# Performance work log

Measured on AMD Instinct MI355X. Metric: run time of the kernel, lower is better.

The kernel has to match this reference:

```python
import jax, jax.numpy as jnp
import numpy as np

N = 100000    # nodes ('paper')
E = 600000    # edges per relation
R = 3         # relations (etypes)
IN = 256      # in_feats
HF = 256      # h_feats
H = 4         # n_heads
D = HF // H   # per-head dim
C = 153       # num_classes
NEG_SLOPE = 0.2


def setup_inputs() -> dict:
    key = jax.random.key(0)
    ks = jax.random.split(key, 14)
    s = 0.05
    x = jax.random.normal(ks[0], (N, IN), jnp.float32)
    src = jax.random.randint(ks[1], (R, E), 0, N, jnp.int32)
    dst = jax.random.randint(ks[2], (R, E), 0, N, jnp.int32)
    # layer 1 params (per relation): fc weight, attn_l, attn_r, bias
    W1 = jax.random.normal(ks[3], (R, IN, HF), jnp.float32) * s
    al1 = jax.random.normal(ks[4], (R, H, D), jnp.float32) * s
    ar1 = jax.random.normal(ks[5], (R, H, D), jnp.float32) * s
    b1 = jax.random.normal(ks[6], (R, HF), jnp.float32) * s
    # layer 2 params
    W2 = jax.random.normal(ks[7], (R, HF, HF), jnp.float32) * s
    al2 = jax.random.normal(ks[8], (R, H, D), jnp.float32) * s
    ar2 = jax.random.normal(ks[9], (R, H, D), jnp.float32) * s
    b2 = jax.random.normal(ks[10], (R, HF), jnp.float32) * s
    # output linear
    Wout = jax.random.normal(ks[11], (HF, C), jnp.float32) * s
    bout = jax.random.normal(ks[12], (C,), jnp.float32) * s
    return {"x": x, "src": src, "dst": dst,
            "W1": W1, "al1": al1, "ar1": ar1, "b1": b1,
            "W2": W2, "al2": al2, "ar2": ar2, "b2": b2,
            "Wout": Wout, "bout": bout}


def _hetero_gat_layer(h, src, dst, W, al, ar, b):
    """HeteroGraphConv over R relations of GATConv, aggregate='sum'.
    h: [N, F_in] -> returns [N, H, D]."""
    acc = jnp.zeros((N, H, D), h.dtype)
    for r in range(R):  # small fixed relation set
        sr, dr = src[r], dst[r]
        feat = (h @ W[r]).reshape(N, H, D)           # projected [N,H,D]
        el = jnp.sum(feat * al[r], axis=-1)          # [N,H]
        er = jnp.sum(feat * ar[r], axis=-1)          # [N,H]
        e = jax.nn.leaky_relu(el[sr] + er[dr], NEG_SLOPE)  # [E,H]
        # edge softmax per destination node, per head
        m = jax.ops.segment_max(e, dr, num_segments=N)     # [N,H]
        a = jnp.exp(e - m[dr])                             # [E,H]
        z = jax.ops.segment_sum(a, dr, num_segments=N)     # [N,H]
        alpha = a / z[dr]                                  # [E,H]
        msg = feat[sr] * alpha[:, :, None]                 # [E,H,D]
        out = jax.ops.segment_sum(msg, dr, num_segments=N) # [N,H,D]
        acc = acc + out + b[r].reshape(1, H, D)
    return acc


def reference(x, src, dst, W1, al1, ar1, b1, W2, al2, ar2, b2, Wout, bout):
    h = _hetero_gat_layer(x, src, dst, W1, al1, ar1, b1).reshape(N, HF)
    h = jax.nn.relu(h)  # apply_each(h, F.relu); dropout is identity in eval
    h = _hetero_gat_layer(h, src, dst, W2, al2, ar2, b2).reshape(N, HF)
    return h @ Wout + bout  # self.linear(h['paper'])
```

## Files before the change

kernel.cpp:

```cpp
#include <hip/hip_runtime.h>
#include <hip/hip_bf16.h>

#define NN 100000
#define EE 600000
#define RR 3
#define INF 256
#define HFF 256
#define NH 4
#define DD 64
#define CC 153
#define NB 98

typedef __attribute__((ext_vector_type(8))) _Float16 f16x8;
typedef __attribute__((ext_vector_type(2))) _Float16 h2f16;
typedef __attribute__((ext_vector_type(4))) float f32x4;

#define GLDS(g, l) __builtin_amdgcn_global_load_lds((const __attribute__((address_space(1))) void*)(g), \
                                                    (__attribute__((address_space(3))) void*)(l), 16, 0, 0)

static __device__ __forceinline__ unsigned short f2h(float x) {
    _Float16 h = (_Float16)x;
    return __builtin_bit_cast(unsigned short, h);
}
static __device__ __forceinline__ float h2f(unsigned short u) {
    return (float)__builtin_bit_cast(_Float16, u);
}

template<int GM>
__global__ __launch_bounds__(256) void mfma_gemm(const unsigned short* __restrict__ A,
                                                 const unsigned short* __restrict__ Bt,
                                                 const float* __restrict__ bias,
                                                 float* __restrict__ C32,
                                                 unsigned short* __restrict__ C16,
                                                 const float* __restrict__ al,
                                                 const float* __restrict__ ar,
                                                 float* __restrict__ el,
                                                 float* __restrict__ er,
                                                 int M) {
    __shared__ __align__(1024) char lds[32768];
    const int tid = threadIdx.x;
    const int lane = tid & 63;
    const int w = tid >> 6;
    const int wr = w >> 1, wc = w & 1;
    const int bm = blockIdx.x * 128;
    const int bn = blockIdx.y * 128;

    f32x4 acc[4][4] = {};

    const int lrow8 = lane >> 3;
    const int cbs = ((lane & 7) << 4) ^ ((lrow8 & 7) << 4);
    const int cbase = w * 8;
    const bool isA = (w < 2);

    const char* gA = (const char*)A;
    const char* gB = (const char*)Bt;

    for (int step = 0; step < 4; ++step) {
        const int k0b = step * 128;
#pragma unroll
        for (int i = 0; i < 8; ++i) {
            int c = cbase + i;
            char* lptr = &lds[c * 1024];
            if (isA) {
                int R = c * 8 + lrow8;
                int grow = bm + R; if (grow >= M) grow = M - 1;
                GLDS(gA + (size_t)grow * 512 + k0b + cbs, lptr);
            } else {
                int nIdx = (c - 16) * 8 + lrow8;
                GLDS(gB + (size_t)(bn + nIdx) * 512 + k0b + cbs, lptr);
            }
        }
        __syncthreads();
#pragma unroll
        for (int kk = 0; kk < 2; ++kk) {
            f16x8 af[4], bfr[4];
            const int o = kk * 64 + ((lane >> 4) << 4);
#pragma unroll
            for (int m = 0; m < 4; ++m) {
                int R = wr * 64 + m * 16 + (lane & 15);
                af[m] = *reinterpret_cast<const f16x8*>(&lds[R * 128 + (o ^ ((R & 7) << 4))]);
            }
#pragma unroll
            for (int n = 0; n < 4; ++n) {
                int Rn = wc * 64 + n * 16 + (lane & 15);
                bfr[n] = *reinterpret_cast<const f16x8*>(&lds[16384 + Rn * 128 + (o ^ ((Rn & 7) << 4))]);
            }
#pragma unroll
            for (int m = 0; m < 4; ++m)
#pragma unroll
                for (int n = 0; n < 4; ++n)
                    acc[m][n] = __builtin_amdgcn_mfma_f32_16x16x32_f16(af[m], bfr[n], acc[m][n], 0, 0, 0);
        }
        __syncthreads();
    }

    const int rb = bm + wr * 64 + ((lane >> 4) << 2);

    if (GM == 0) {
        const int cb2 = bn + wc * 64 + (lane & 15);
#pragma unroll
        for (int m = 0; m < 4; ++m)
#pragma unroll
            for (int n = 0; n < 4; ++n) {
                int col = cb2 + n * 16;
                if (col < CC) {
                    float bb = bias[col];
#pragma unroll
                    for (int j = 0; j < 4; ++j) {
                        int row = rb + m * 16 + j;
                        if (row < M) C32[(size_t)row * CC + col] = acc[m][n][j] + bb;
                    }
                }
            }
    } else {
        const int c0 = bn + wc * 64;
        const int rh = c0 >> 6;
        const int rw = rh >> 2;
        const int h  = rh & 3;
        float alv[4], arv[4];
#pragma unroll
        for (int n = 0; n < 4; ++n) {
            alv[n] = al[rh * 64 + n * 16 + (lane & 15)];
            arv[n] = ar[rh * 64 + n * 16 + (lane & 15)];
        }
#pragma unroll
        for (int m = 0; m < 4; ++m)
#pragma unroll
            for (int j = 0; j < 4; ++j) {
                float pl = acc[m][0][j] * alv[0] + acc[m][1][j] * alv[1]
                         + acc[m][2][j] * alv[2] + acc[m][3][j] * alv[3];
                float pr = acc[m][0][j] * arv[0] + acc[m][1][j] * arv[1]
                         + acc[m][2][j] * arv[2] + acc[m][3][j] * arv[3];
#pragma unroll
                for (int o2 = 1; o2 < 16; o2 <<= 1) {
                    pl += __shfl_xor(pl, o2);
                    pr += __shfl_xor(pr, o2);
                }
                int row = rb + m * 16 + j;
                if ((lane & 15) == 0 && row < M) {
                    el[(size_t)rw * NN * 4 + row * 4 + h] = pl;
                    er[(size_t)rw * NN * 4 + row * 4 + h] = pr;
                }
            }
        __syncthreads();
        unsigned short* l16 = (unsigned short*)lds;
#pragma unroll
        for (int m = 0; m < 4; ++m)
#pragma unroll
            for (int n = 0; n < 4; ++n)
#pragma unroll
                for (int j = 0; j < 4; ++j) {
                    int row = wr * 64 + m * 16 + ((lane >> 4) << 2) + j;
                    int colb = (wc * 64 + n * 16 + (lane & 15)) * 2;
                    int addr = row * 256 + (colb ^ (((row >> 2) & 7) << 5));
                    l16[addr >> 1] = f2h(acc[m][n][j]);
                }
        __syncthreads();
        const int rblk = bn >> 8;
        const int bnc  = bn & 255;
        const size_t NFE = (size_t)NN * 256;
#pragma unroll
        for (int i = 0; i < 8; ++i) {
            int seg = w * 8 + i;
            int row = seg * 4 + (lane >> 4);
            int colb = (lane & 15) * 16;
            int addr = row * 256 + (colb ^ (((row >> 2) & 7) << 5));
            uint4 v = *reinterpret_cast<const uint4*>(&lds[addr]);
            int grow = bm + row;
            if (grow < M) {
                unsigned short* gp = C16 + (size_t)rblk * NFE + (size_t)grow * 256 + bnc + (lane & 15) * 8;
                *reinterpret_cast<uint4*>(gp) = v;
            }
        }
    }
}

__global__ __launch_bounds__(256) void f2h4(const float* __restrict__ in,
                                            unsigned short* __restrict__ out, int n4) {
    int i = blockIdx.x * 256 + threadIdx.x;
    if (i >= n4) return;
    float4 v = reinterpret_cast<const float4*>(in)[i];
    ushort4 o;
    o.x = f2h(v.x); o.y = f2h(v.y); o.z = f2h(v.z); o.w = f2h(v.w);
    reinterpret_cast<ushort4*>(out)[i] = o;
}

__global__ __launch_bounds__(256) void wt_kernel(const float* __restrict__ W,
                                                 unsigned short* __restrict__ Wt) {
    int idx = blockIdx.x * 256 + threadIdx.x;
    if (idx >= RR * 65536) return;
    int r = idx >> 16, rem = idx & 65535;
    int n = rem >> 8, k = rem & 255;
    Wt[idx] = f2h(W[(r << 16) + (k << 8) + n]);
}

__global__ __launch_bounds__(256) void wout_kernel(const float* __restrict__ Wout,
                                                   unsigned short* __restrict__ Wt) {
    int idx = blockIdx.x * 256 + threadIdx.x;
    if (idx >= 65536) return;
    int n = idx >> 8, k = idx & 255;
    Wt[idx] = (n < CC) ? f2h(Wout[k * CC + n]) : (unsigned short)0;
}

__global__ __launch_bounds__(256) void hist_kernel(const int* __restrict__ dst,
                                                   int* __restrict__ deg) {
    int i = blockIdx.x * 256 + threadIdx.x;
    if (i >= RR * EE) return;
    int r = i / EE;
    atomicAdd(&deg[r * NN + dst[i]], 1);
}

__global__ __launch_bounds__(256) void scan_block(const int* __restrict__ deg,
                                                  int* __restrict__ rowptr,
                                                  int* __restrict__ bsum) {
    __shared__ int sh[256];
    int r = blockIdx.y, b = blockIdx.x, t = threadIdx.x;
    int base = b * 1024;
    int v[4];
#pragma unroll
    for (int j = 0; j < 4; ++j) {
        int idx = base + t * 4 + j;
        v[j] = (idx < NN) ? deg[r * NN + idx] : 0;
    }
    int tsum = v[0] + v[1] + v[2] + v[3];
    sh[t] = tsum;
    __syncthreads();
    for (int off = 1; off < 256; off <<= 1) {
        int x = (t >= off) ? sh[t - off] : 0;
        __syncthreads();
        sh[t] += x;
        __syncthreads();
    }
    int run = sh[t] - tsum;
#pragma unroll
    for (int j = 0; j < 4; ++j) {
        int idx = base + t * 4 + j;
        if (idx < NN) rowptr[r * (NN + 1) + idx] = run;
        run += v[j];
    }
    if (t == 255) bsum[r * NB + b] = run;
}

__global__ void scan_bsum(int* __restrict__ bsum, int* __restrict__ rowptr) {
    int r = threadIdx.x;
    if (r >= RR) return;
    int run = 0;
    for (int b = 0; b < NB; ++b) {
        int x = bsum[r * NB + b];
        bsum[r * NB + b] = run;
        run += x;
    }
    rowptr[r * (NN + 1) + NN] = run;
}

__global__ __launch_bounds__(256) void add_off(int* __restrict__ rowptr,
                                               const int* __restrict__ bsum) {
    int r = blockIdx.y, b = blockIdx.x, t = threadIdx.x;
    int o = bsum[r * NB + b];
#pragma unroll
    for (int j = 0; j < 4; ++j) {
        int idx = b * 1024 + t * 4 + j;
        if (idx < NN) rowptr[r * (NN + 1) + idx] += o;
    }
}

__global__ __launch_bounds__(256) void fill_kernel(const int* __restrict__ src,
                                                   const int* __restrict__ dst,
                                                   const int* __restrict__ rowptr,
                                                   int* __restrict__ cursor,
                                                   int* __restrict__ csrc) {
    int i = blockIdx.x * 256 + threadIdx.x;
    if (i >= RR * EE) return;
    int r = i / EE;
    int d = dst[i], s = src[i];
    int pos = rowptr[r * (NN + 1) + d] + atomicAdd(&cursor[r * NN + d], 1);
    csrc[(size_t)r * EE + pos] = s;
}

template<int RELU>
__global__ __launch_bounds__(256) void agg3_kernel(const int* __restrict__ csrc,
                                                   const int* __restrict__ rowptr,
                                                   const float* __restrict__ el,
                                                   const float* __restrict__ er,
                                                   const unsigned short* __restrict__ feat,
                                                   const float* __restrict__ brel,
                                                   unsigned short* __restrict__ hout) {
    int wid = (blockIdx.x * 256 + threadIdx.x) >> 6;
    int lane = threadIdx.x & 63;
    if (wid >= NN) return;
    int d = wid;
    int h = lane >> 4;
    int f0 = lane * 4;

    float4 bA = *reinterpret_cast<const float4*>(brel + f0);
    float4 bB = *reinterpret_cast<const float4*>(brel + 256 + f0);
    float4 bC = *reinterpret_cast<const float4*>(brel + 512 + f0);
    float4 cur = make_float4(bA.x + bB.x + bC.x, bA.y + bB.y + bC.y,
                             bA.z + bB.z + bC.z, bA.w + bB.w + bC.w);

#pragma unroll
    for (int r = 0; r < RR; ++r) {
        int p0 = rowptr[r * (NN + 1) + d], p1 = rowptr[r * (NN + 1) + d + 1];
        if (p0 == p1) continue;
        float erd = er[(size_t)r * NN * 4 + d * 4 + h];
        const float* elr = el + (size_t)r * NN * 4;
        const unsigned short* fr = feat + (size_t)r * NN * 256;
        const int* cs = csrc + (size_t)r * EE;

        h2f16 aA01 = (h2f16)0, aA23 = (h2f16)0;
        h2f16 aB01 = (h2f16)0, aB23 = (h2f16)0;
        float zs = 0.f;
        int last = p1 - 1;
        for (int p = p0; p < p1; p += 4) {
            int q1 = p + 1 <= last ? p + 1 : last;
            int q2 = p + 2 <= last ? p + 2 : last;
            int q3 = p + 3 <= last ? p + 3 : last;
            int s0 = cs[p], s1 = cs[q1], s2 = cs[q2], s3 = cs[q3];
            uint2 fA = *reinterpret_cast<const uint2*>(fr + (size_t)s0 * 256 + f0);
            uint2 fB = *reinterpret_cast<const uint2*>(fr + (size_t)s1 * 256 + f0);
            uint2 fC = *reinterpret_cast<const uint2*>(fr + (size_t)s2 * 256 + f0);
            uint2 fD = *reinterpret_cast<const uint2*>(fr + (size_t)s3 * 256 + f0);
            float v0 = elr[s0 * 4 + h] + erd;
            float v1 = elr[s1 * 4 + h] + erd;
            float v2 = elr[s2 * 4 + h] + erd;
            float v3 = elr[s3 * 4 + h] + erd;
            v0 = v0 > 0.f ? v0 : 0.2f * v0;
            v1 = v1 > 0.f ? v1 : 0.2f * v1;
            v2 = v2 > 0.f ? v2 : 0.2f * v2;
            v3 = v3 > 0.f ? v3 : 0.2f * v3;
            float w0 = __expf(v0);
            float w1 = (p + 1 <= last) ? __expf(v1) : 0.f;
            float w2 = (p + 2 <= last) ? __expf(v2) : 0.f;
            float w3 = (p + 3 <= last) ? __expf(v3) : 0.f;
            zs += (w0 + w1) + (w2 + w3);
            _Float16 h0 = (_Float16)w0, h1 = (_Float16)w1;
            _Float16 h2 = (_Float16)w2, h3 = (_Float16)w3;
            h2f16 wp0 = (h2f16){h0, h0}, wp1 = (h2f16){h1, h1};
            h2f16 wp2 = (h2f16){h2, h2}, wp3 = (h2f16){h3, h3};
            aA01 += wp0 * __builtin_bit_cast(h2f16, fA.x);
            aA23 += wp0 * __builtin_bit_cast(h2f16, fA.y);
            aB01 += wp1 * __builtin_bit_cast(h2f16, fB.x);
            aB23 += wp1 * __builtin_bit_cast(h2f16, fB.y);
            aA01 += wp2 * __builtin_bit_cast(h2f16, fC.x);
            aA23 += wp2 * __builtin_bit_cast(h2f16, fC.y);
            aB01 += wp3 * __builtin_bit_cast(h2f16, fD.x);
            aB23 += wp3 * __builtin_bit_cast(h2f16, fD.y);
        }
        float inv = 1.f / zs;
        cur.x += ((float)aA01[0] + (float)aB01[0]) * inv;
        cur.y += ((float)aA01[1] + (float)aB01[1]) * inv;
        cur.z += ((float)aA23[0] + (float)aB23[0]) * inv;
        cur.w += ((float)aA23[1] + (float)aB23[1]) * inv;
    }
    if (RELU) {
        cur.x = fmaxf(cur.x, 0.f); cur.y = fmaxf(cur.y, 0.f);
        cur.z = fmaxf(cur.z, 0.f); cur.w = fmaxf(cur.w, 0.f);
    }
    ushort4 o;
    o.x = f2h(cur.x); o.y = f2h(cur.y); o.z = f2h(cur.z); o.w = f2h(cur.w);
    *reinterpret_cast<ushort4*>(hout + (size_t)d * 256 + f0) = o;
}

extern "C" void kernel_launch(void* const* d_in, const int* in_sizes, int n_in,
                              void* d_out, int out_size, void* d_ws, size_t ws_size,
                              hipStream_t stream) {
    const float* x    = (const float*)d_in[0];
    const int*   src  = (const int*)d_in[1];
    const int*   dst  = (const int*)d_in[2];
    const float* W1   = (const float*)d_in[3];
    const float* al1  = (const float*)d_in[4];
    const float* ar1  = (const float*)d_in[5];
    const float* b1   = (const float*)d_in[6];
    const float* W2   = (const float*)d_in[7];
    const float* al2  = (const float*)d_in[8];
    const float* ar2  = (const float*)d_in[9];
    const float* b2   = (const float*)d_in[10];
    const float* Wout = (const float*)d_in[11];
    const float* bout = (const float*)d_in[12];
    float* out = (float*)d_out;

    char* base = (char*)d_ws;
    size_t off = 0;
    auto alloc = [&](size_t bytes) -> char* {
        char* p = base + off;
        off = (off + bytes + 255) & ~(size_t)255;
        return p;
    };
    size_t NF = (size_t)NN * HFF;
    unsigned short* feath = (unsigned short*)alloc(RR * NF * 2);
    float* el   = (float*)alloc((size_t)RR * NN * NH * 4);
    float* er   = (float*)alloc((size_t)RR * NN * NH * 4);
    int* deg    = (int*)alloc((size_t)RR * NN * 4 * 2);
    int* cursor = deg + (size_t)RR * NN;
    int* rowptr = (int*)alloc((size_t)RR * (NN + 1) * 4);
    int* bsum   = (int*)alloc((size_t)RR * NB * 4);
    int* csrc   = (int*)alloc((size_t)RR * EE * 4);
    unsigned short* xh    = (unsigned short*)alloc(NF * 2);
    unsigned short* wth   = (unsigned short*)alloc((size_t)2 * RR * 65536 * 2);
    unsigned short* wouth = (unsigned short*)alloc((size_t)65536 * 2);

    int n4Blocks = (int)((NF / 4 + 255) / 256);
    int reBlocks = (RR * EE + 255) / 256;
    int aggBlocks = (NN * 64 + 255) / 256;
    dim3 pgrid((NN + 127) / 128, 6);
    dim3 ogrid((NN + 127) / 128, 2);

    hipMemsetAsync(deg, 0, (size_t)RR * NN * sizeof(int) * 2, stream);
    hist_kernel<<<reBlocks, 256, 0, stream>>>(dst, deg);
    scan_block<<<dim3(NB, RR), 256, 0, stream>>>(deg, rowptr, bsum);
    scan_bsum<<<1, 64, 0, stream>>>(bsum, rowptr);
    add_off<<<dim3(NB, RR), 256, 0, stream>>>(rowptr, bsum);
    fill_kernel<<<reBlocks, 256, 0, stream>>>(src, dst, rowptr, cursor, csrc);

    f2h4<<<n4Blocks, 256, 0, stream>>>(x, xh, (int)(NF / 4));
    wt_kernel<<<(RR * 65536) / 256, 256, 0, stream>>>(W1, wth);
    wt_kernel<<<(RR * 65536) / 256, 256, 0, stream>>>(W2, wth + (size_t)RR * 65536);
    wout_kernel<<<65536 / 256, 256, 0, stream>>>(Wout, wouth);

    for (int layer = 0; layer < 2; ++layer) {
        const float* al = layer ? al2 : al1;
        const float* ar = layer ? ar2 : ar1;
        const float* b  = layer ? b2 : b1;
        const unsigned short* wl = wth + (size_t)layer * RR * 65536;

        mfma_gemm<1><<<pgrid, 256, 0, stream>>>(xh, wl, nullptr,
                                                nullptr, feath, al, ar, el, er, NN);
        if (layer == 0)
            agg3_kernel<1><<<aggBlocks, 256, 0, stream>>>(csrc, rowptr, el, er, feath, b, xh);
        else
            agg3_kernel<0><<<aggBlocks, 256, 0, stream>>>(csrc, rowptr, el, er, feath, b, xh);
    }

    mfma_gemm<0><<<ogrid, 256, 0, stream>>>(xh, wouth, bout, out, nullptr,
                                            nullptr, nullptr, nullptr, nullptr, NN);
}
```

Baseline: 813.9 us.

## Precompute per-edge attention weights in separate kernel and unroll aggregation by eight

Adds a per-edge kernel that computes the leaky-relu and exp attention weights for all four heads once, in CSR order, and stores them as fp16. The aggregation kernel then reads these weights instead of recomputing el/er gathers and exponentials in every lane, and unrolls the edge loop to eight with four accumulator pairs to expose more memory-level parallelism. The GEMM grid is also swapped so the N-column tiles vary fastest, which improves reuse of A rows across the column blocks. In exchange it adds extra edge-sized buffers (cdst, weights), one extra launch per layer, and rounds the weights to fp16 before they are summed into the normalizer.

```diff
diff --git a/kernel.cpp b/kernel.cpp
--- a/kernel.cpp
+++ b/kernel.cpp
@@ -42,8 +42,8 @@
     const int lane = tid & 63;
     const int w = tid >> 6;
     const int wr = w >> 1, wc = w & 1;
-    const int bm = blockIdx.x * 128;
-    const int bn = blockIdx.y * 128;
+    const int bm = blockIdx.y * 128;
+    const int bn = blockIdx.x * 128;
 
     f32x4 acc[4][4] = {};
 
@@ -268,20 +268,46 @@
                                                    const int* __restrict__ dst,
                                                    const int* __restrict__ rowptr,
                                                    int* __restrict__ cursor,
-                                                   int* __restrict__ csrc) {
+                                                   int* __restrict__ csrc,
+                                                   int* __restrict__ cdst) {
     int i = blockIdx.x * 256 + threadIdx.x;
     if (i >= RR * EE) return;
     int r = i / EE;
     int d = dst[i], s = src[i];
     int pos = rowptr[r * (NN + 1) + d] + atomicAdd(&cursor[r * NN + d], 1);
     csrc[(size_t)r * EE + pos] = s;
+    cdst[(size_t)r * EE + pos] = d;
+}
+
+__global__ __launch_bounds__(256) void wk_kernel(const int* __restrict__ csrc,
+                                                 const int* __restrict__ cdst,
+                                                 const float* __restrict__ el,
+                                                 const float* __restrict__ er,
+                                                 unsigned short* __restrict__ wt) {
+    int p = blockIdx.x * 256 + threadIdx.x;
+    if (p >= EE) return;
+    int r = blockIdx.y;
+    size_t e = (size_t)r * EE + p;
+    int s = csrc[e], d = cdst[e];
+    const float* elr = el + (size_t)r * NN * 4;
+    const float* err2 = er + (size_t)r * NN * 4;
+    float4 le = *reinterpret_cast<const float4*>(elr + s * 4);
+    float4 re = *reinterpret_cast<const float4*>(err2 + d * 4);
+    float v0 = le.x + re.x, v1 = le.y + re.y, v2 = le.z + re.z, v3 = le.w + re.w;
+    v0 = v0 > 0.f ? v0 : 0.2f * v0;
+    v1 = v1 > 0.f ? v1 : 0.2f * v1;
+    v2 = v2 > 0.f ? v2 : 0.2f * v2;
+    v3 = v3 > 0.f ? v3 : 0.2f * v3;
+    ushort4 o;
+    o.x = f2h(__expf(v0)); o.y = f2h(__expf(v1));
+    o.z = f2h(__expf(v2)); o.w = f2h(__expf(v3));
+    *reinterpret_cast<ushort4*>(wt + e * 4) = o;
 }
 
 template<int RELU>
 __global__ __launch_bounds__(256) void agg3_kernel(const int* __restrict__ csrc,
                                                    const int* __restrict__ rowptr,
-                                                   const float* __restrict__ el,
-                                                   const float* __restrict__ er,
+                                                   const unsigned short* __restrict__ wt,
                                                    const unsigned short* __restrict__ feat,
                                                    const float* __restrict__ brel,
                                                    unsigned short* __restrict__ hout) {
@@ -302,55 +328,38 @@
     for (int r = 0; r < RR; ++r) {
         int p0 = rowptr[r * (NN + 1) + d], p1 = rowptr[r * (NN + 1) + d + 1];
         if (p0 == p1) continue;
-        float erd = er[(size_t)r * NN * 4 + d * 4 + h];
-        const float* elr = el + (size_t)r * NN * 4;
         const unsigned short* fr = feat + (size_t)r * NN * 256;
         const int* cs = csrc + (size_t)r * EE;
-
-        h2f16 aA01 = (h2f16)0, aA23 = (h2f16)0;
-        h2f16 aB01 = (h2f16)0, aB23 = (h2f16)0;
+        const unsigned short* wtr = wt + (size_t)r * EE * 4;
+
+        h2f16 a01[4] = {};
+        h2f16 a23[4] = {};
         float zs = 0.f;
         int last = p1 - 1;
-        for (int p = p0; p < p1; p += 4) {
-            int q1 = p + 1 <= last ? p + 1 : last;
-            int q2 = p + 2 <= last ? p + 2 : last;
-            int q3 = p + 3 <= last ? p + 3 : last;
-            int s0 = cs[p], s1 = cs[q1], s2 = cs[q2], s3 = cs[q3];
-            uint2 fA = *reinterpret_cast<const uint2*>(fr + (size_t)s0 * 256 + f0);
-            uint2 fB = *reinterpret_cast<const uint2*>(fr + (size_t)s1 * 256 + f0);
-            uint2 fC = *reinterpret_cast<const uint2*>(fr + (size_t)s2 * 256 + f0);
-            uint2 fD = *reinterpret_cast<const uint2*>(fr + (size_t)s3 * 256 + f0);
-            float v0 = elr[s0 * 4 + h] + erd;
-            float v1 = elr[s1 * 4 + h] + erd;
-            float v2 = elr[s2 * 4 + h] + erd;
-            float v3 = elr[s3 * 4 + h] + erd;
-            v0 = v0 > 0.f ? v0 : 0.2f * v0;
-            v1 = v1 > 0.f ? v1 : 0.2f * v1;
-            v2 = v2 > 0.f ? v2 : 0.2f * v2;
-            v3 = v3 > 0.f ? v3 : 0.2f * v3;
-            float w0 = __expf(v0);
-            float w1 = (p + 1 <= last) ? __expf(v1) : 0.f;
-            float w2 = (p + 2 <= last) ? __expf(v2) : 0.f;
-            float w3 = (p + 3 <= last) ? __expf(v3) : 0.f;
-            zs += (w0 + w1) + (w2 + w3);
-            _Float16 h0 = (_Float16)w0, h1 = (_Float16)w1;
-            _Float16 h2 = (_Float16)w2, h3 = (_Float16)w3;
-            h2f16 wp0 = (h2f16){h0, h0}, wp1 = (h2f16){h1, h1};
-            h2f16 wp2 = (h2f16){h2, h2}, wp3 = (h2f16){h3, h3};
-            aA01 += wp0 * __builtin_bit_cast(h2f16, fA.x);
-            aA23 += wp0 * __builtin_bit_cast(h2f16, fA.y);
-            aB01 += wp1 * __builtin_bit_cast(h2f16, fB.x);
-            aB23 += wp1 * __builtin_bit_cast(h2f16, fB.y);
-            aA01 += wp2 * __builtin_bit_cast(h2f16, fC.x);
-            aA23 += wp2 * __builtin_bit_cast(h2f16, fC.y);
-            aB01 += wp3 * __builtin_bit_cast(h2f16, fD.x);
-            aB23 += wp3 * __builtin_bit_cast(h2f16, fD.y);
+        for (int p = p0; p < p1; p += 8) {
+#pragma unroll
+            for (int k = 0; k < 8; ++k) {
+                int q = (p + k <= last) ? p + k : last;
+                int s = cs[q];
+                uint2 fv = *reinterpret_cast<const uint2*>(fr + (size_t)s * 256 + f0);
+                unsigned short wu = wtr[q * 4 + h];
+                if (p + k > last) wu = 0;
+                _Float16 wh = __builtin_bit_cast(_Float16, wu);
+                zs += (float)wh;
+                h2f16 wp = (h2f16){wh, wh};
+                a01[k & 3] += wp * __builtin_bit_cast(h2f16, fv.x);
+                a23[k & 3] += wp * __builtin_bit_cast(h2f16, fv.y);
+            }
         }
         float inv = 1.f / zs;
-        cur.x += ((float)aA01[0] + (float)aB01[0]) * inv;
-        cur.y += ((float)aA01[1] + (float)aB01[1]) * inv;
-        cur.z += ((float)aA23[0] + (float)aB23[0]) * inv;
-        cur.w += ((float)aA23[1] + (float)aB23[1]) * inv;
+        float s01a = (float)a01[0][0] + (float)a01[1][0] + (float)a01[2][0] + (float)a01[3][0];
+        float s01b = (float)a01[0][1] + (float)a01[1][1] + (float)a01[2][1] + (float)a01[3][1];
+        float s23a = (float)a23[0][0] + (float)a23[1][0] + (float)a23[2][0] + (float)a23[3][0];
+        float s23b = (float)a23[0][1] + (float)a23[1][1] + (float)a23[2][1] + (float)a23[3][1];
+        cur.x += s01a * inv;
+        cur.y += s01b * inv;
+        cur.z += s23a * inv;
+        cur.w += s23b * inv;
     }
     if (RELU) {
         cur.x = fmaxf(cur.x, 0.f); cur.y = fmaxf(cur.y, 0.f);
@@ -395,6 +404,8 @@
     int* rowptr = (int*)alloc((size_t)RR * (NN + 1) * 4);
     int* bsum   = (int*)alloc((size_t)RR * NB * 4);
     int* csrc   = (int*)alloc((size_t)RR * EE * 4);
+    int* cdst   = (int*)alloc((size_t)RR * EE * 4);
+    unsigned short* wedge = (unsigned short*)alloc((size_t)RR * EE * 4 * 2);
     unsigned short* xh    = (unsigned short*)alloc(NF * 2);
     unsigned short* wth   = (unsigned short*)alloc((size_t)2 * RR * 65536 * 2);
     unsigned short* wouth = (unsigned short*)alloc((size_t)65536 * 2);
@@ -402,15 +413,16 @@
     int n4Blocks = (int)((NF / 4 + 255) / 256);
     int reBlocks = (RR * EE + 255) / 256;
     int aggBlocks = (NN * 64 + 255) / 256;
-    dim3 pgrid((NN + 127) / 128, 6);
-    dim3 ogrid((NN + 127) / 128, 2);
+    dim3 pgrid(6, (NN + 127) / 128);
+    dim3 ogrid(2, (NN + 127) / 128);
+    dim3 wgrid((EE + 255) / 256, RR);
 
     hipMemsetAsync(deg, 0, (size_t)RR * NN * sizeof(int) * 2, stream);
     hist_kernel<<<reBlocks, 256, 0, stream>>>(dst, deg);
     scan_block<<<dim3(NB, RR), 256, 0, stream>>>(deg, rowptr, bsum);
     scan_bsum<<<1, 64, 0, stream>>>(bsum, rowptr);
     add_off<<<dim3(NB, RR), 256, 0, stream>>>(rowptr, bsum);
-    fill_kernel<<<reBlocks, 256, 0, stream>>>(src, dst, rowptr, cursor, csrc);
+    fill_kernel<<<reBlocks, 256, 0, stream>>>(src, dst, rowptr, cursor, csrc, cdst);
 
     f2h4<<<n4Blocks, 256, 0, stream>>>(x, xh, (int)(NF / 4));
     wt_kernel<<<(RR * 65536) / 256, 256, 0, stream>>>(W1, wth);
@@ -425,10 +437,11 @@
 
         mfma_gemm<1><<<pgrid, 256, 0, stream>>>(xh, wl, nullptr,
                                                 nullptr, feath, al, ar, el, er, NN);
+        wk_kernel<<<wgrid, 256, 0, stream>>>(csrc, cdst, el, er, wedge);
         if (layer == 0)
-            agg3_kernel<1><<<aggBlocks, 256, 0, stream>>>(csrc, rowptr, el, er, feath, b, xh);
+            agg3_kernel<1><<<aggBlocks, 256, 0, stream>>>(csrc, rowptr, wedge, feath, b, xh);
         else
-            agg3_kernel<0><<<aggBlocks, 256, 0, stream>>>(csrc, rowptr, el, er, feath, b, xh);
+            agg3_kernel<0><<<aggBlocks, 256, 0, stream>>>(csrc, rowptr, wedge, feath, b, xh);
     }
 
     mfma_gemm<0><<<ogrid, 256, 0, stream>>>(xh, wouth, bout, out, nullptr,
```

Result: slower. 859.1 us (+5.6%).
